# Kernel optimization log

Measured on AMD Instinct MI355X. Metric: run time of the kernel, lower is better.

## Reference

```python
import jax, jax.numpy as jnp
import numpy as np

K = 9        # kNN neighbors (ViG default kernel_size=9)
EPS = 1e-5   # BatchNorm eps


def _bn2d(x, gamma, beta):
    # training-mode BatchNorm2d over (B,H,W) per channel; x: [B,C,H,W]
    mean = jnp.mean(x, axis=(0, 2, 3), keepdims=True)
    var = jnp.var(x, axis=(0, 2, 3), keepdims=True)
    g = gamma.reshape(1, -1, 1, 1)
    b = beta.reshape(1, -1, 1, 1)
    return g * (x - mean) * jax.lax.rsqrt(var + EPS) + b


def setup_inputs() -> dict:
    key = jax.random.key(0)
    B, C, H, W = 8, 96, 56, 56
    oup = 192
    ks = jax.random.split(key, 8)
    sc = 0.05
    return {
        "x": jax.random.normal(ks[0], (B, C, H, W), dtype=jnp.float32),
        "W_fc1": jax.random.normal(ks[1], (C, C), dtype=jnp.float32) * sc,
        "b_fc1": jnp.zeros((C,), jnp.float32),
        "g_bn1": jnp.ones((C,), jnp.float32),
        "be_bn1": jnp.zeros((C,), jnp.float32),
        "W_edge": jax.random.normal(ks[2], (2 * C, 2 * C), dtype=jnp.float32) * sc,
        "b_edge": jnp.zeros((2 * C,), jnp.float32),
        "g_bne": jnp.ones((2 * C,), jnp.float32),
        "be_bne": jnp.zeros((2 * C,), jnp.float32),
        "W_fc2": jax.random.normal(ks[3], (2 * C, C), dtype=jnp.float32) * sc,
        "b_fc2": jnp.zeros((C,), jnp.float32),
        "g_bn2": jnp.ones((C,), jnp.float32),
        "be_bn2": jnp.zeros((C,), jnp.float32),
        "g_sabn": jnp.ones((C,), jnp.float32),
        "be_sabn": jnp.zeros((C,), jnp.float32),
        "W_dw": jax.random.normal(ks[4], (oup, C, 3, 3), dtype=jnp.float32) * sc,
        "b_dw": jnp.zeros((oup,), jnp.float32),
        "g_dwbn": jnp.ones((oup,), jnp.float32),
        "be_dwbn": jnp.zeros((oup,), jnp.float32),
    }


def reference(x, W_fc1, b_fc1, g_bn1, be_bn1, W_edge, b_edge, g_bne, be_bne,
              W_fc2, b_fc2, g_bn2, be_bn2, g_sabn, be_sabn,
              W_dw, b_dw, g_dwbn, be_dwbn):
    B, C, H, W = x.shape
    N = H * W
    shortcut = x

    # --- Grapher.fc1: 1x1 conv + BN ---
    y = jnp.einsum('bchw,cd->bdhw', x, W_fc1) + b_fc1[None, :, None, None]
    y = _bn2d(y, g_bn1, be_bn1)

    # --- dynamic kNN graph over flattened tokens ---
    ft = y.reshape(B, C, N).transpose(0, 2, 1)            # [B,N,C]
    sq = jnp.sum(ft * ft, axis=-1)                        # [B,N]
    dist = sq[:, :, None] - 2.0 * jnp.einsum('bnc,bmc->bnm', ft, ft) + sq[:, None, :]
    _, idx = jax.lax.top_k(-dist, K)                      # [B,N,K] nearest neighbors

    # --- EdgeConv: max_k act(BN(W [x_i, x_j - x_i])) ---
    x_j = jnp.take_along_axis(ft[:, :, None, :], idx[..., None], axis=1)  # [B,N,K,C]
    x_i = ft[:, :, None, :]                               # [B,N,1,C]
    e = jnp.concatenate([jnp.broadcast_to(x_i, x_j.shape), x_j - x_i], axis=-1)  # [B,N,K,2C]
    e = jnp.einsum('bnkc,cd->bnkd', e, W_edge) + b_edge
    m = jnp.mean(e, axis=(0, 1, 2))
    v = jnp.var(e, axis=(0, 1, 2))
    e = g_bne * (e - m) * jax.lax.rsqrt(v + EPS) + be_bne
    e = jax.nn.relu(e)
    g = jnp.max(e, axis=2)                                # [B,N,2C] max-aggregation

    # --- Grapher.fc2: 1x1 conv + BN, residual ---
    g = jnp.einsum('bnc,cd->bnd', g, W_fc2) + b_fc2       # [B,N,C]
    g = g.transpose(0, 2, 1).reshape(B, C, H, W)
    g = _bn2d(g, g_bn2, be_bn2)
    y = g + shortcut

    # --- SAEncoder: BN + ReLU ---
    y = jax.nn.relu(_bn2d(y, g_sabn, be_sabn))

    # --- convdw: 3x3 stride-2 conv + BN + ReLU ---
    y = jax.lax.conv_general_dilated(
        y, W_dw, window_strides=(2, 2), padding=((1, 1), (1, 1)),
        dimension_numbers=('NCHW', 'OIHW', 'NCHW')) + b_dw[None, :, None, None]
    y = jax.nn.relu(_bn2d(y, g_dwbn, be_dwbn))
    return y
```

## Files before the change

kernel.cpp:

```cpp
#include <hip/hip_runtime.h>
#include <math.h>

#define B_   8
#define C_   96
#define C2_  192
#define N_   3136
#define R_   25088
#define OUP_ 192
#define HO_  28
#define NO_  784
#define EPS_ 1e-5f
#define QS2  128
#define CAP3 64

typedef short bf16x8 __attribute__((ext_vector_type(8)));
typedef float f32x4  __attribute__((ext_vector_type(4)));

__device__ __forceinline__ int swz16(int i) { return (i & ~15) | ((i & 15) ^ ((i >> 4) & 7)); }

__global__ __launch_bounds__(512) void k_fc1_d(const float* __restrict__ x,
                                               const float* __restrict__ W1,
                                               const float* __restrict__ b1,
                                               double* __restrict__ yd) {
    __shared__ double Wl[96 * 48];
    int tid = threadIdx.x;
    int rl = tid & 255, h = tid >> 8;
    int dbase = blockIdx.y * 48;
    for (int q = tid; q < 96 * 48; q += 512) {
        int c = q / 48, dd = q % 48;
        Wl[c * 48 + dd] = (double)W1[c * 96 + dbase + dd];
    }
    __syncthreads();
    int r = blockIdx.x * 256 + rl;
    int b = r / N_;
    int n = r - b * N_;
    double acc[24];
#pragma unroll
    for (int i = 0; i < 24; i++) acc[i] = 0.0;
    const float* xp = x + (size_t)b * C_ * N_ + n;
    for (int c = 0; c < 96; ++c) {
        double xv = (double)xp[(size_t)c * N_];
        const double* w = &Wl[c * 48 + h * 24];
#pragma unroll
        for (int i = 0; i < 24; ++i) acc[i] += xv * w[i];
    }
    int d0 = dbase + h * 24;
#pragma unroll
    for (int i = 0; i < 24; i++) {
        int d = d0 + i;
        yd[((size_t)b * C_ + d) * N_ + n] = acc[i] + (double)b1[d];
    }
}

__global__ __launch_bounds__(256) void k_stats_chan_d(const double* __restrict__ src,
                                                      double* __restrict__ partial) {
    int c = blockIdx.x;
    int chunk = blockIdx.y;
    const int SPLIT = 16;
    double s = 0.0, ss = 0.0;
    for (int j = chunk * 256 + threadIdx.x; j < R_; j += SPLIT * 256) {
        int b = j / N_, n = j - b * N_;
        double v = src[((size_t)b * C_ + c) * N_ + n];
        s += v;
        ss += v * v;
    }
    __shared__ double red[8];
    for (int off = 32; off; off >>= 1) {
        s += __shfl_down(s, off, 64);
        ss += __shfl_down(ss, off, 64);
    }
    int lane = threadIdx.x & 63, w = threadIdx.x >> 6;
    if (lane == 0) { red[w * 2] = s; red[w * 2 + 1] = ss; }
    __syncthreads();
    if (threadIdx.x == 0) {
        s = red[0] + red[2] + red[4] + red[6];
        ss = red[1] + red[3] + red[5] + red[7];
        partial[(c * SPLIT + chunk) * 2] = s;
        partial[(c * SPLIT + chunk) * 2 + 1] = ss;
    }
}

__global__ void k_stats_reduce_d(const double* __restrict__ partial, double* __restrict__ stats) {
    int c = blockIdx.x * blockDim.x + threadIdx.x;
    if (c >= 96) return;
    double s = 0.0, ss = 0.0;
    for (int k = 0; k < 16; k++) {
        s += partial[(c * 16 + k) * 2];
        ss += partial[(c * 16 + k) * 2 + 1];
    }
    double m = s / (double)R_;
    double var = ss / (double)R_ - m * m;
    stats[c * 2] = m;
    stats[c * 2 + 1] = 1.0 / sqrt(var + 1e-5);
}

__global__ __launch_bounds__(256) void k_stats_chan(const float* __restrict__ src,
                                                    float* __restrict__ partial,
                                                    int Cn, int Nsp, int total) {
    int c = blockIdx.x;
    int chunk = blockIdx.y;
    int SPLIT = gridDim.y;
    float s = 0.f, ss = 0.f;
    for (int j = chunk * 256 + threadIdx.x; j < total; j += SPLIT * 256) {
        int b = j / Nsp, n = j - b * Nsp;
        float v = src[((size_t)b * Cn + c) * Nsp + n];
        s += v;
        ss += v * v;
    }
    __shared__ float red[8];
    for (int off = 32; off; off >>= 1) {
        s += __shfl_down(s, off, 64);
        ss += __shfl_down(ss, off, 64);
    }
    int lane = threadIdx.x & 63, w = threadIdx.x >> 6;
    if (lane == 0) { red[w * 2] = s; red[w * 2 + 1] = ss; }
    __syncthreads();
    if (threadIdx.x == 0) {
        s = red[0] + red[2] + red[4] + red[6];
        ss = red[1] + red[3] + red[5] + red[7];
        partial[(c * SPLIT + chunk) * 2] = s;
        partial[(c * SPLIT + chunk) * 2 + 1] = ss;
    }
}

__global__ void k_stats_reduce(const float* __restrict__ partial, float* __restrict__ stats,
                               int Cn, int SPLIT, float invcount) {
    int c = blockIdx.x * blockDim.x + threadIdx.x;
    if (c >= Cn) return;
    float s = 0.f, ss = 0.f;
    for (int k = 0; k < SPLIT; k++) {
        s += partial[(c * SPLIT + k) * 2];
        ss += partial[(c * SPLIT + k) * 2 + 1];
    }
    float m = s * invcount;
    float var = ss * invcount - m * m;
    stats[c * 2] = m;
    stats[c * 2 + 1] = 1.0f / sqrtf(var + EPS_);
}

__global__ __launch_bounds__(256) void k_stats_reduce_b2(const float* __restrict__ partial,
                                                         float* __restrict__ stats,
                                                         float invcount) {
    int c = blockIdx.x;
    float s = 0.f, ss = 0.f;
    for (int k = threadIdx.x; k < 784; k += 256) {
        s  += partial[(size_t)k * 384 + c];
        ss += partial[(size_t)k * 384 + 192 + c];
    }
    __shared__ float red[8];
    for (int off = 32; off; off >>= 1) {
        s += __shfl_down(s, off, 64);
        ss += __shfl_down(ss, off, 64);
    }
    int lane = threadIdx.x & 63, w = threadIdx.x >> 6;
    if (lane == 0) { red[w * 2] = s; red[w * 2 + 1] = ss; }
    __syncthreads();
    if (threadIdx.x == 0) {
        s = red[0] + red[2] + red[4] + red[6];
        ss = red[1] + red[3] + red[5] + red[7];
        float m = s * invcount;
        float var = ss * invcount - m * m;
        stats[c * 2] = m;
        stats[c * 2 + 1] = 1.0f / sqrtf(var + EPS_);
    }
}

__global__ __launch_bounds__(256) void k_bn1_tr(const double* __restrict__ yd,
                                                const double* __restrict__ stats,
                                                const float* __restrict__ g,
                                                const float* __restrict__ be,
                                                float* __restrict__ ftc,
                                                double* __restrict__ ftp64,
                                                unsigned short* __restrict__ fspH,
                                                double* __restrict__ sq64) {
    __shared__ double tile[64 * 97];
    __shared__ double dsq[64][4];
    int b = blockIdx.y;
    int n0 = blockIdx.x * 64;
    int tid = threadIdx.x;
    int n = tid & 63, w = tid >> 6;
    for (int k = 0; k < 24; ++k) {
        int c = k * 4 + w;
        size_t gi = ((size_t)b * C_ + c) * N_ + n0 + n;
        double m = stats[c * 2], rs = stats[c * 2 + 1];
        double v = (double)g[c] * (yd[gi] - m) * rs + (double)be[c];
        ftc[gi] = (float)v;
        tile[n * 97 + c] = v;
    }
    __syncthreads();
    int p = n, q = w;
    double vals[24];
    double s = 0.0;
    const double* lp = &tile[p * 97 + q * 24];
#pragma unroll
    for (int m2 = 0; m2 < 24; ++m2) { vals[m2] = lp[m2]; s += vals[m2] * vals[m2]; }
    dsq[p][q] = s;
    double* dst = ftp64 + ((size_t)b * N_ + n0 + p) * C_ + q * 24;
#pragma unroll
    for (int m2 = 0; m2 < 24; m2 += 2) *(double2*)&dst[m2] = make_double2(vals[m2], vals[m2 + 1]);
    unsigned* hdst = (unsigned*)(fspH + ((size_t)b * N_ + n0 + p) * QS2);
#pragma unroll
    for (int m2 = 0; m2 < 24; m2 += 2) {
        unsigned u0 = __float_as_uint((float)vals[m2]);
        unsigned u1 = __float_as_uint((float)vals[m2 + 1]);
        unsigned h0 = (u0 + 0x7fffu + ((u0 >> 16) & 1u)) >> 16;
        unsigned h1 = (u1 + 0x7fffu + ((u1 >> 16) & 1u)) >> 16;
        hdst[q * 12 + (m2 >> 1)] = h0 | (h1 << 16);
    }
    __syncthreads();
    if (tid < 64) {
        double tot = dsq[tid][0] + dsq[tid][1] + dsq[tid][2] + dsq[tid][3];
        sq64[(size_t)b * N_ + n0 + tid] = tot;
        float t32 = (float)(-0.5 * tot);
        unsigned u0 = __float_as_uint(t32);
        unsigned h0 = (u0 + 0x7fffu + ((u0 >> 16) & 1u)) >> 16;
        float resid = t32 - __uint_as_float(h0 << 16);
        unsigned u1 = __float_as_uint(resid);
        unsigned h1 = (u1 + 0x7fffu + ((u1 >> 16) & 1u)) >> 16;
        unsigned* hd = (unsigned*)(fspH + ((size_t)b * N_ + n0 + tid) * QS2);
        hd[48] = h0 | (h1 << 16);
#pragma unroll
        for (int k2 = 49; k2 < 64; ++k2) hd[k2] = 0u;
    }
}

__global__ __launch_bounds__(256) void k_dist_min(const unsigned short* __restrict__ fspH,
                                                  unsigned short* __restrict__ cminG) {
    __shared__ __align__(16) char lds[32768];
    int b = blockIdx.z, half = blockIdx.y;
    int q0 = blockIdx.x * 64;
    int tid = threadIdx.x, w = tid >> 6, l = tid & 63;
    int ch0 = half * 25;
    int nch = half ? 24 : 25;
    const int koff = (l >> 4) * 8;

    {
        const uint4* qsrc = (const uint4*)(fspH + ((size_t)b * N_ + q0) * QS2);
        const uint4* csrc = (const uint4*)(fspH + ((size_t)b * N_ + ch0 * 64) * QS2);
        uint4* qb = (uint4*)(lds + 16384);
        uint4* cb = (uint4*)lds;
        for (int i = tid; i < 1024; i += 256) { qb[swz16(i)] = qsrc[i]; cb[swz16(i)] = csrc[i]; }
    }
    __syncthreads();
    bf16x8 Bq[4];
    {
        const unsigned short* Ql = (const unsigned short*)(lds + 16384);
        int qr = w * 16 + (l & 15);
#pragma unroll
        for (int s = 0; s < 3; ++s) {
            int col = (s * 4 + (l >> 4)) ^ (qr & 7);
            Bq[s] = *(const bf16x8*)&Ql[qr * QS2 + col * 8];
        }
        bf16x8 z = {0, 0, 0, 0, 0, 0, 0, 0};
        if ((l >> 4) == 0) { z[0] = (short)0x3F80; z[1] = (short)0x3F80; }
        Bq[3] = z;
    }
    __syncthreads();

    int cur = 0;
    for (int t = 0; t < nch; ++t) {
        int chg = ch0 + t;
        bool pf = (t < nch - 1);
        uint4 st0, st1, st2, st3;
        if (pf) {
            const uint4* src = (const uint4*)(fspH + ((size_t)b * N_ + (chg + 1) * 64) * QS2);
            st0 = src[tid]; st1 = src[tid + 256]; st2 = src[tid + 512]; st3 = src[tid + 768];
        }
        const unsigned short* Bc = (const unsigned short*)(lds + cur * 16384);
        f32x4 acc[4];
#pragma unroll
        for (int ct = 0; ct < 4; ++ct) acc[ct] = (f32x4){0.f, 0.f, 0.f, 0.f};
#pragma unroll
        for (int s = 0; s < 4; ++s) {
#pragma unroll
            for (int ct = 0; ct < 4; ++ct) {
                int cr = ct * 16 + (l & 15);
                int col = (s * 4 + (l >> 4)) ^ (cr & 7);
                bf16x8 Ac = *(const bf16x8*)&Bc[cr * QS2 + col * 8];
                acc[ct] = __builtin_amdgcn_mfma_f32_16x16x32_bf16(Ac, Bq[s], acc[ct], 0, 0, 0);
            }
        }
        float mx = -1e30f;
#pragma unroll
        for (int ct = 0; ct < 4; ++ct)
#pragma unroll
            for (int j = 0; j < 4; ++j) mx = fmaxf(mx, acc[ct][j]);
        mx = fmaxf(mx, __shfl_xor(mx, 16, 64));
        mx = fmaxf(mx, __shfl_xor(mx, 32, 64));
        if (l < 16) {
            float dmin = -2.f * mx;
            unsigned u = __float_as_uint(dmin);
            unsigned ku = u ^ (0x80000000u | (unsigned)((int)u >> 31));
            cminG[((size_t)(b * N_ + q0 + w * 16 + l)) * 49 + chg] = (unsigned short)(ku >> 16);
        }
        if (pf) {
            uint4* dst = (uint4*)(lds + (cur ^ 1) * 16384);
            dst[swz16(tid)] = st0;
            dst[swz16(tid + 256)] = st1;
            dst[swz16(tid + 512)] = st2;
            dst[swz16(tid + 768)] = st3;
        }
        __syncthreads();
        cur ^= 1;
    }
}

__global__ __launch_bounds__(256) void k_t9(const unsigned short* __restrict__ cminG,
                                            float* __restrict__ thr2f,
                                            unsigned* __restrict__ poolCnt) {
    int q = blockIdx.x * 256 + threadIdx.x;
    if (q >= R_) return;
    const unsigned short* p = cminG + (size_t)q * 49;
    unsigned short top[9];
#pragma unroll
    for (int j = 0; j < 9; ++j) top[j] = 0xFFFFu;
    for (int i = 0; i < 49; ++i) {
        unsigned short v = p[i];
        if (v < top[8]) {
            top[8] = v;
#pragma unroll
            for (int j = 8; j >= 1; --j)
                if (top[j] < top[j - 1]) { unsigned short tt = top[j]; top[j] = top[j - 1]; top[j - 1] = tt; }
        }
    }
    unsigned ku = ((unsigned)top[8] << 16) | 0xFFFFu;
    float f = (ku & 0x80000000u) ? __uint_as_float(ku ^ 0x80000000u) : __uint_as_float(~ku);
    float t9 = f + fabsf(f) * 0.008f + 0.75f;
    thr2f[q] = -0.5f * t9;
    poolCnt[q] = 0u;
}

__global__ __launch_bounds__(256) void k_dist_cmp(const unsigned short* __restrict__ fspH,
                                                  const float* __restrict__ thr2f,
                                                  unsigned short* __restrict__ poolC,
                                                  unsigned* __restrict__ poolCnt) {
    __shared__ __align__(16) char lds[32768];
    int b = blockIdx.z, half = blockIdx.y;
    int q0 = blockIdx.x * 64;
    int tid = threadIdx.x, w = tid >> 6, l = tid & 63;
    int ch0 = half * 25;
    int nch = half ? 24 : 25;
    const int koff = (l >> 4) * 8;
    int qg = b * N_ + q0 + w * 16 + (l & 15);
    float thr2r = thr2f[qg];

    {
        const uint4* qsrc = (const uint4*)(fspH + ((size_t)b * N_ + q0) * QS2);
        const uint4* csrc = (const uint4*)(fspH + ((size_t)b * N_ + ch0 * 64) * QS2);
        uint4* qb = (uint4*)(lds + 16384);
        uint4* cb = (uint4*)lds;
        for (int i = tid; i < 1024; i += 256) { qb[swz16(i)] = qsrc[i]; cb[swz16(i)] = csrc[i]; }
    }
    __syncthreads();
    bf16x8 Bq[4];
    {
        const unsigned short* Ql = (const unsigned short*)(lds + 16384);
        int qr = w * 16 + (l & 15);
#pragma unroll
        for (int s = 0; s < 3; ++s) {
            int col = (s * 4 + (l >> 4)) ^ (qr & 7);
            Bq[s] = *(const bf16x8*)&Ql[qr * QS2 + col * 8];
        }
        bf16x8 z = {0, 0, 0, 0, 0, 0, 0, 0};
        if ((l >> 4) == 0) { z[0] = (short)0x3F80; z[1] = (short)0x3F80; }
        Bq[3] = z;
    }
    __syncthreads();

    int cur = 0;
    for (int t = 0; t < nch; ++t) {
        int chg = ch0 + t;
        int c0 = chg * 64;
        bool pf = (t < nch - 1);
        uint4 st0, st1, st2, st3;
        if (pf) {
            const uint4* src = (const uint4*)(fspH + ((size_t)b * N_ + (chg + 1) * 64) * QS2);
            st0 = src[tid]; st1 = src[tid + 256]; st2 = src[tid + 512]; st3 = src[tid + 768];
        }
        const unsigned short* Bc = (const unsigned short*)(lds + cur * 16384);
        f32x4 acc[4];
#pragma unroll
        for (int ct = 0; ct < 4; ++ct) acc[ct] = (f32x4){0.f, 0.f, 0.f, 0.f};
#pragma unroll
        for (int s = 0; s < 4; ++s) {
#pragma unroll
            for (int ct = 0; ct < 4; ++ct) {
                int cr = ct * 16 + (l & 15);
                int col = (s * 4 + (l >> 4)) ^ (cr & 7);
                bf16x8 Ac = *(const bf16x8*)&Bc[cr * QS2 + col * 8];
                acc[ct] = __builtin_amdgcn_mfma_f32_16x16x32_bf16(Ac, Bq[s], acc[ct], 0, 0, 0);
            }
        }
#pragma unroll
        for (int ct = 0; ct < 4; ++ct)
#pragma unroll
            for (int j = 0; j < 4; ++j) {
                if (acc[ct][j] >= thr2r) {
                    unsigned pos = atomicAdd(&poolCnt[qg], 1u);
                    if (pos < (unsigned)CAP3)
                        poolC[(size_t)qg * CAP3 + pos] = (unsigned short)(c0 + ct * 16 + (l >> 4) * 4 + j);
                }
            }
        if (pf) {
            uint4* dst = (uint4*)(lds + (cur ^ 1) * 16384);
            dst[swz16(tid)] = st0;
            dst[swz16(tid + 256)] = st1;
            dst[swz16(tid + 512)] = st2;
            dst[swz16(tid + 768)] = st3;
        }
        __syncthreads();
        cur ^= 1;
    }
}

__global__ __launch_bounds__(256) void k_rerank_d(const unsigned short* __restrict__ poolC,
                                                  const unsigned* __restrict__ poolCnt,
                                                  const double* __restrict__ ftp64,
                                                  const double* __restrict__ sq64,
                                                  int* __restrict__ idx) {
    int tid = threadIdx.x;
    int wv = tid >> 6, l = tid & 63;
    int rr = blockIdx.x * 4 + wv;
    int b = rr / N_;
    int cnt = (int)poolCnt[rr];
    if (cnt > CAP3) cnt = CAP3;
    int e = l & 3;
    double qreg[24];
    {
        const double* qb = ftp64 + (size_t)rr * C_ + e * 24;
#pragma unroll
        for (int m = 0; m < 24; ++m) qreg[m] = qb[m];
    }
    double dv[4];
    int jv[4];
#pragma unroll
    for (int gG = 0; gG < 4; ++gG) { dv[gG] = 1e300; jv[gG] = 0x7fffffff; }
#pragma unroll
    for (int gG = 0; gG < 4; ++gG) {
        if (gG * 16 >= cnt) break;
        int ci = gG * 16 + (l >> 2);
        bool valid = ci < cnt;
        int j = valid ? (int)poolC[(size_t)rr * CAP3 + ci] : 0;
        const double* cb = ftp64 + ((size_t)b * N_ + j) * C_ + e * 24;
        double p = 0.0;
#pragma unroll
        for (int m = 0; m < 24; ++m) p += qreg[m] * cb[m];
        p += __shfl_xor(p, 1, 64);
        p += __shfl_xor(p, 2, 64);
        if (valid) {
            dv[gG] = sq64[(size_t)b * N_ + j] - 2.0 * p;
            jv[gG] = j;
        }
    }
#pragma unroll
    for (int r = 0; r < 9; ++r) {
        double dm = dv[0]; int jm = jv[0];
#pragma unroll
        for (int gG = 1; gG < 4; ++gG)
            if (dv[gG] < dm || (dv[gG] == dm && jv[gG] < jm)) { dm = dv[gG]; jm = jv[gG]; }
#pragma unroll
        for (int off = 1; off <= 32; off <<= 1) {
            double od = __shfl_xor(dm, off, 64);
            int oj = __shfl_xor(jm, off, 64);
            if (od < dm || (od == dm && oj < jm)) { dm = od; jm = oj; }
        }
        if (l == 0) idx[(size_t)rr * 9 + r] = jm;
#pragma unroll
        for (int gG = 0; gG < 4; ++gG)
            if (jv[gG] == jm) dv[gG] = 1e300;
    }
}

__global__ __launch_bounds__(512) void k_gemm_uv2(const float* __restrict__ ftc,
                                                  const float* __restrict__ We,
                                                  const float* __restrict__ beb,
                                                  float* __restrict__ u,
                                                  float* __restrict__ v) {
    __shared__ float Wl[2][96 * 48];
    int tid = threadIdx.x;
    int rl = tid & 255, h = tid >> 8;
    int dbase = blockIdx.y * 48;
    for (int q = tid; q < 96 * 48; q += 512) {
        int c = q / 48, dd = q % 48;
        float wb = We[(96 + c) * C2_ + dbase + dd];
        Wl[1][q] = wb;
        Wl[0][q] = We[c * C2_ + dbase + dd] - wb;
    }
    __syncthreads();
    int r = blockIdx.x * 256 + rl;
    int b = r / N_, n = r - b * N_;
    float a0[24], a1[24];
#pragma unroll
    for (int i = 0; i < 24; i++) { a0[i] = 0.f; a1[i] = 0.f; }
    const float* xp = ftc + (size_t)b * C_ * N_ + n;
    for (int c = 0; c < 96; ++c) {
        float xv = xp[(size_t)c * N_];
        const float4* w40 = (const float4*)&Wl[0][c * 48 + h * 24];
        const float4* w41 = (const float4*)&Wl[1][c * 48 + h * 24];
#pragma unroll
        for (int i = 0; i < 6; ++i) {
            float4 w0 = w40[i], w1 = w41[i];
            a0[i * 4 + 0] += xv * w0.x; a0[i * 4 + 1] += xv * w0.y;
            a0[i * 4 + 2] += xv * w0.z; a0[i * 4 + 3] += xv * w0.w;
            a1[i * 4 + 0] += xv * w1.x; a1[i * 4 + 1] += xv * w1.y;
            a1[i * 4 + 2] += xv * w1.z; a1[i * 4 + 3] += xv * w1.w;
        }
    }
    int d0 = dbase + h * 24;
    float* up = u + (size_t)r * C2_ + d0;
    float* vp = v + (size_t)r * C2_ + d0;
#pragma unroll
    for (int i = 0; i < 6; ++i) {
        float4 ou, ov;
        ou.x = a0[i * 4 + 0] + beb[d0 + i * 4 + 0];
        ou.y = a0[i * 4 + 1] + beb[d0 + i * 4 + 1];
        ou.z = a0[i * 4 + 2] + beb[d0 + i * 4 + 2];
        ou.w = a0[i * 4 + 3] + beb[d0 + i * 4 + 3];
        ov.x = a1[i * 4 + 0]; ov.y = a1[i * 4 + 1];
        ov.z = a1[i * 4 + 2]; ov.w = a1[i * 4 + 3];
        ((float4*)up)[i] = ou;
        ((float4*)vp)[i] = ov;
    }
}

__global__ __launch_bounds__(192) void k_bne_stats(const float* __restrict__ u,
                                                   const float* __restrict__ v,
                                                   const int* __restrict__ idx,
                                                   float* __restrict__ partial) {
    int d = threadIdx.x;
    int row0 = blockIdx.x * 32;
    int b = row0 / N_;
    float s = 0.f, ss = 0.f;
    for (int r = 0; r < 32; ++r) {
        int row = row0 + r;
        float ud = u[(size_t)row * C2_ + d];
        const int* ip = idx + (size_t)row * 9;
#pragma unroll
        for (int k = 0; k < 9; k++) {
            int j = ip[k];
            float e = ud + v[((size_t)b * N_ + j) * C2_ + d];
            s += e;
            ss += e * e;
        }
    }
    partial[(size_t)blockIdx.x * 384 + d] = s;
    partial[(size_t)blockIdx.x * 384 + 192 + d] = ss;
}

__global__ __launch_bounds__(192) void k_edge_fc2(const float* __restrict__ u,
                                                  const float* __restrict__ v,
                                                  const int* __restrict__ idx,
                                                  const float* __restrict__ statsE,
                                                  const float* __restrict__ ge,
                                                  const float* __restrict__ bee,
                                                  const float* __restrict__ W2,
                                                  const float* __restrict__ b2,
                                                  float* __restrict__ out2) {
    __shared__ float gl[16][C2_];
    __shared__ float g2[C_][16];
    int tid = threadIdx.x;
    int row0 = blockIdx.x * 16;
    int b = row0 / N_;
    int n0 = row0 - b * N_;
    {
        int d = tid;
        float m = statsE[d * 2], rs = statsE[d * 2 + 1];
        float ga = ge[d], bb = bee[d];
        for (int r = 0; r < 16; ++r) {
            int row = row0 + r;
            float ud = u[(size_t)row * C2_ + d];
            const int* ip = idx + (size_t)row * 9;
            float gm = 0.f;
#pragma unroll
            for (int k = 0; k < 9; k++) {
                int j = ip[k];
                float e = ud + v[((size_t)b * N_ + j) * C2_ + d];
                float val = ga * (e - m) * rs + bb;
                gm = fmaxf(gm, val);
            }
            gl[r][d] = gm;
        }
    }
    __syncthreads();
    {
        int rr = tid / 24;
        int dq = tid % 24;
        for (int rep = 0; rep < 2; ++rep) {
            int r = rr + rep * 8;
            float4 acc = *(const float4*)&b2[dq * 4];
            for (int d = 0; d < C2_; ++d) {
                float gv = gl[r][d];
                float4 w = *(const float4*)&W2[d * C_ + dq * 4];
                acc.x += gv * w.x;
                acc.y += gv * w.y;
                acc.z += gv * w.z;
                acc.w += gv * w.w;
            }
            g2[dq * 4 + 0][r] = acc.x;
            g2[dq * 4 + 1][r] = acc.y;
            g2[dq * 4 + 2][r] = acc.z;
            g2[dq * 4 + 3][r] = acc.w;
        }
    }
    __syncthreads();
    for (int q = tid; q < 96 * 4; q += 192) {
        int dd = q / 4, part = q % 4;
        float4 val = *(const float4*)&g2[dd][part * 4];
        *(float4*)&out2[((size_t)b * C_ + dd) * N_ + n0 + part * 4] = val;
    }
}

__global__ __launch_bounds__(256) void k_bn2_add_st(const float* __restrict__ out2,
                                                    const float* __restrict__ x,
                                                    const float* __restrict__ stats,
                                                    const float* __restrict__ g,
                                                    const float* __restrict__ be,
                                                    float* __restrict__ t,
                                                    float* __restrict__ partial) {
    int c = blockIdx.x;
    int chunk = blockIdx.y;
    const int SPLIT = 16;
    float m = stats[c * 2], rs = stats[c * 2 + 1];
    float ga = g[c], bb = be[c];
    float s = 0.f, ss = 0.f;
    for (int j = chunk * 256 + threadIdx.x; j < R_; j += SPLIT * 256) {
        int b = j / N_, n = j - b * N_;
        size_t i = ((size_t)b * C_ + c) * N_ + n;
        float tv = ga * (out2[i] - m) * rs + bb + x[i];
        t[i] = tv;
        s += tv;
        ss += tv * tv;
    }
    __shared__ float red[8];
    for (int off = 32; off; off >>= 1) {
        s += __shfl_down(s, off, 64);
        ss += __shfl_down(ss, off, 64);
    }
    int lane = threadIdx.x & 63, w = threadIdx.x >> 6;
    if (lane == 0) { red[w * 2] = s; red[w * 2 + 1] = ss; }
    __syncthreads();
    if (threadIdx.x == 0) {
        s = red[0] + red[2] + red[4] + red[6];
        ss = red[1] + red[3] + red[5] + red[7];
        partial[(c * SPLIT + chunk) * 2] = s;
        partial[(c * SPLIT + chunk) * 2 + 1] = ss;
    }
}

__global__ __launch_bounds__(256) void k_sabn_relu(const float* __restrict__ t,
                                                   const float* __restrict__ stats,
                                                   const float* __restrict__ g,
                                                   const float* __restrict__ be,
                                                   float* __restrict__ s) {
    int i = blockIdx.x * 256 + threadIdx.x;
    if (i >= B_ * C_ * N_) return;
    int c = (i / N_) % C_;
    s[i] = fmaxf(g[c] * (t[i] - stats[c * 2]) * stats[c * 2 + 1] + be[c], 0.f);
}

__global__ __launch_bounds__(256) void k_conv(const float* __restrict__ s,
                                              const float* __restrict__ Wd,
                                              const float* __restrict__ bd,
                                              float* __restrict__ z) {
    __shared__ float Wl[96 * 9 * 16];
    int b = blockIdx.z;
    int oc0 = blockIdx.y * 16;
    int p = blockIdx.x * 256 + threadIdx.x;
    for (int i = threadIdx.x; i < 96 * 9 * 16; i += 256) {
        int oc = i & 15;
        int icq = i >> 4;
        Wl[i] = Wd[(size_t)(oc0 + oc) * 864 + icq];
    }
    __syncthreads();
    if (p >= NO_) return;
    int oh = p / HO_, ow = p % HO_;
    float acc[16];
#pragma unroll
    for (int i = 0; i < 16; i++) acc[i] = 0.f;
    int ih0 = oh * 2 - 1, iw0 = ow * 2 - 1;
    const float* sb = s + (size_t)b * C_ * N_;
    for (int ic = 0; ic < 96; ++ic) {
        const float* sp = sb + (size_t)ic * N_;
        float in[9];
#pragma unroll
        for (int kh = 0; kh < 3; kh++) {
            int ih = ih0 + kh;
            bool okh = (unsigned)ih < 56u;
#pragma unroll
            for (int kw = 0; kw < 3; kw++) {
                int iw = iw0 + kw;
                bool ok = okh && ((unsigned)iw < 56u);
                in[kh * 3 + kw] = ok ? sp[ih * 56 + iw] : 0.f;
            }
        }
#pragma unroll
        for (int q = 0; q < 9; q++) {
            float iv = in[q];
            const float4* w4 = (const float4*)&Wl[(ic * 9 + q) * 16];
#pragma unroll
            for (int j = 0; j < 4; j++) {
                float4 w = w4[j];
                acc[j * 4 + 0] += iv * w.x;
                acc[j * 4 + 1] += iv * w.y;
                acc[j * 4 + 2] += iv * w.z;
                acc[j * 4 + 3] += iv * w.w;
            }
        }
    }
#pragma unroll
    for (int i = 0; i < 16; i++)
        z[((size_t)b * OUP_ + oc0 + i) * NO_ + p] = acc[i] + bd[oc0 + i];
}

__global__ __launch_bounds__(256) void k_out(const float* __restrict__ z,
                                             const float* __restrict__ stats,
                                             const float* __restrict__ g,
                                             const float* __restrict__ be,
                                             float* __restrict__ out) {
    int i = blockIdx.x * 256 + threadIdx.x;
    if (i >= B_ * OUP_ * NO_) return;
    int c = (i / NO_) % OUP_;
    out[i] = fmaxf(g[c] * (z[i] - stats[c * 2]) * stats[c * 2 + 1] + be[c], 0.f);
}

extern "C" void kernel_launch(void* const* d_in, const int* in_sizes, int n_in,
                              void* d_out, int out_size, void* d_ws, size_t ws_size,
                              hipStream_t stream) {
    const float* x     = (const float*)d_in[0];
    const float* W_fc1 = (const float*)d_in[1];
    const float* b_fc1 = (const float*)d_in[2];
    const float* g_bn1 = (const float*)d_in[3];
    const float* be_bn1= (const float*)d_in[4];
    const float* W_edge= (const float*)d_in[5];
    const float* b_edge= (const float*)d_in[6];
    const float* g_bne = (const float*)d_in[7];
    const float* be_bne= (const float*)d_in[8];
    const float* W_fc2 = (const float*)d_in[9];
    const float* b_fc2 = (const float*)d_in[10];
    const float* g_bn2 = (const float*)d_in[11];
    const float* be_bn2= (const float*)d_in[12];
    const float* g_sabn= (const float*)d_in[13];
    const float* be_sabn=(const float*)d_in[14];
    const float* W_dw  = (const float*)d_in[15];
    const float* b_dw  = (const float*)d_in[16];
    const float* g_dwbn= (const float*)d_in[17];
    const float* be_dwbn=(const float*)d_in[18];

    char* base = (char*)d_ws;
    float*  ftc   = (float*)(base + 0);
    float*  sbuf  = (float*)(base + 0);
    double* ftp64 = (double*)(base + 9633792);
    float*  uu    = (float*)(base + 9633792);
    double* yd    = (double*)(base + 28901376);
    float*  vv    = (float*)(base + 28901376);
    unsigned short* fspH = (unsigned short*)(base + 48168960);
    float*  out2  = (float*)(base + 48168960);
    unsigned short* poolC = (unsigned short*)(base + 57802752);
    float*  tbuf  = (float*)(base + 57802752);
    double* sq64  = (double*)(base + 67436544);
    int*    idx   = (int*)(base + 67637248);
    unsigned* poolCnt = (unsigned*)(base + 68540416);
    float*  thr2f = (float*)(base + 68640768);
    float*  partial = (float*)(base + 68741120);
    double* partiald = (double*)(base + 68741120);
    double* stats1d = (double*)(base + 69945344);
    float*  statsE  = (float*)(base + 69946880);
    float*  stats2  = (float*)(base + 69948416);
    float*  statsS  = (float*)(base + 69949952);
    float*  statsD  = (float*)(base + 69951488);
    float*  zbuf  = (float*)(base + 69953024);
    unsigned short* cminG = (unsigned short*)(base + 69953024);

    k_fc1_d<<<dim3(98, 2), 512, 0, stream>>>(x, W_fc1, b_fc1, yd);
    k_stats_chan_d<<<dim3(96, 16), 256, 0, stream>>>(yd, partiald);
    k_stats_reduce_d<<<1, 256, 0, stream>>>(partiald, stats1d);
    k_bn1_tr<<<dim3(49, B_), 256, 0, stream>>>(yd, stats1d, g_bn1, be_bn1, ftc, ftp64, fspH, sq64);

    k_dist_min<<<dim3(49, 2, B_), 256, 0, stream>>>(fspH, cminG);
    k_t9<<<98, 256, 0, stream>>>(cminG, thr2f, poolCnt);
    k_dist_cmp<<<dim3(49, 2, B_), 256, 0, stream>>>(fspH, thr2f, poolC, poolCnt);
    k_rerank_d<<<6272, 256, 0, stream>>>(poolC, poolCnt, ftp64, sq64, idx);

    k_gemm_uv2<<<dim3(98, 4), 512, 0, stream>>>(ftc, W_edge, b_edge, uu, vv);

    k_bne_stats<<<784, 192, 0, stream>>>(uu, vv, idx, partial);
    k_stats_reduce_b2<<<192, 256, 0, stream>>>(partial, statsE, 1.0f / 225792.0f);
    k_edge_fc2<<<1568, 192, 0, stream>>>(uu, vv, idx, statsE, g_bne, be_bne, W_fc2, b_fc2, out2);

    k_stats_chan<<<dim3(96, 16), 256, 0, stream>>>(out2, partial, 96, N_, R_);
    k_stats_reduce<<<1, 256, 0, stream>>>(partial, stats2, 96, 16, 1.0f / (float)R_);
    k_bn2_add_st<<<dim3(96, 16), 256, 0, stream>>>(out2, x, stats2, g_bn2, be_bn2, tbuf, partial);
    k_stats_reduce<<<1, 256, 0, stream>>>(partial, statsS, 96, 16, 1.0f / (float)R_);
    k_sabn_relu<<<9408, 256, 0, stream>>>(tbuf, statsS, g_sabn, be_sabn, sbuf);

    k_conv<<<dim3(4, 12, 8), 256, 0, stream>>>(sbuf, W_dw, b_dw, zbuf);
    k_stats_chan<<<dim3(192, 8), 256, 0, stream>>>(zbuf, partial, 192, NO_, 6272);
    k_stats_reduce<<<1, 256, 0, stream>>>(partial, statsD, 192, 8, 1.0f / 6272.0f);
    k_out<<<4705, 256, 0, stream>>>(zbuf, statsD, g_dwbn, be_dwbn, (float*)d_out);
}
```

Measured before the change: 590.4 us.

## Fuse kNN threshold passes, fold BN stats into producers, fuse SA-BN into conv

Merges the kNN min-distance pass, the top-9 threshold kernel and the candidate-compare pass into one kernel. Each block computes its own per-chunk minima in LDS, derives the threshold, then re-walks the same chunks to collect candidates, which removes the cminG/thr2f round trips and two launches. The fc2 edge kernel now emits per-block BN2 partial sums, and the conv kernel applies SA-BN+ReLU on the fly and emits BN partials for the output stats. This drops the separate stats-channel passes and the sbuf write. Trade-offs: the conv now uses 8 output channels per block, doubling input re-reads, and the fused kNN kernel streams the candidates twice from global memory inside a single kernel.

```diff
diff --git a/kernel.cpp b/kernel.cpp
--- a/kernel.cpp
+++ b/kernel.cpp
@@ -94,35 +94,6 @@
     stats[c * 2 + 1] = 1.0 / sqrt(var + 1e-5);
 }
 
-__global__ __launch_bounds__(256) void k_stats_chan(const float* __restrict__ src,
-                                                    float* __restrict__ partial,
-                                                    int Cn, int Nsp, int total) {
-    int c = blockIdx.x;
-    int chunk = blockIdx.y;
-    int SPLIT = gridDim.y;
-    float s = 0.f, ss = 0.f;
-    for (int j = chunk * 256 + threadIdx.x; j < total; j += SPLIT * 256) {
-        int b = j / Nsp, n = j - b * Nsp;
-        float v = src[((size_t)b * Cn + c) * Nsp + n];
-        s += v;
-        ss += v * v;
-    }
-    __shared__ float red[8];
-    for (int off = 32; off; off >>= 1) {
-        s += __shfl_down(s, off, 64);
-        ss += __shfl_down(ss, off, 64);
-    }
-    int lane = threadIdx.x & 63, w = threadIdx.x >> 6;
-    if (lane == 0) { red[w * 2] = s; red[w * 2 + 1] = ss; }
-    __syncthreads();
-    if (threadIdx.x == 0) {
-        s = red[0] + red[2] + red[4] + red[6];
-        ss = red[1] + red[3] + red[5] + red[7];
-        partial[(c * SPLIT + chunk) * 2] = s;
-        partial[(c * SPLIT + chunk) * 2 + 1] = ss;
-    }
-}
-
 __global__ void k_stats_reduce(const float* __restrict__ partial, float* __restrict__ stats,
                                int Cn, int SPLIT, float invcount) {
     int c = blockIdx.x * blockDim.x + threadIdx.x;
@@ -138,14 +109,14 @@
     stats[c * 2 + 1] = 1.0f / sqrtf(var + EPS_);
 }
 
-__global__ __launch_bounds__(256) void k_stats_reduce_b2(const float* __restrict__ partial,
-                                                         float* __restrict__ stats,
-                                                         float invcount) {
+__global__ __launch_bounds__(256) void k_stats_reduce_g(const float* __restrict__ partial,
+                                                        float* __restrict__ stats,
+                                                        int Cn, int NB, float invcount) {
     int c = blockIdx.x;
     float s = 0.f, ss = 0.f;
-    for (int k = threadIdx.x; k < 784; k += 256) {
-        s  += partial[(size_t)k * 384 + c];
-        ss += partial[(size_t)k * 384 + 192 + c];
+    for (int k = threadIdx.x; k < NB; k += 256) {
+        s  += partial[(size_t)k * 2 * Cn + c];
+        ss += partial[(size_t)k * 2 * Cn + Cn + c];
     }
     __shared__ float red[8];
     for (int off = 32; off; off >>= 1) {
@@ -172,7 +143,8 @@
                                                 float* __restrict__ ftc,
                                                 double* __restrict__ ftp64,
                                                 unsigned short* __restrict__ fspH,
-                                                double* __restrict__ sq64) {
+                                                double* __restrict__ sq64,
+                                                unsigned* __restrict__ poolCnt) {
     __shared__ double tile[64 * 97];
     __shared__ double dsq[64][4];
     int b = blockIdx.y;
@@ -211,6 +183,7 @@
     if (tid < 64) {
         double tot = dsq[tid][0] + dsq[tid][1] + dsq[tid][2] + dsq[tid][3];
         sq64[(size_t)b * N_ + n0 + tid] = tot;
+        poolCnt[(size_t)b * N_ + n0 + tid] = 0u;
         float t32 = (float)(-0.5 * tot);
         unsigned u0 = __float_as_uint(t32);
         unsigned h0 = (u0 + 0x7fffu + ((u0 >> 16) & 1u)) >> 16;
@@ -224,27 +197,27 @@
     }
 }
 
-__global__ __launch_bounds__(256) void k_dist_min(const unsigned short* __restrict__ fspH,
-                                                  unsigned short* __restrict__ cminG) {
-    __shared__ __align__(16) char lds[32768];
+__global__ __launch_bounds__(256) void k_dist5(const unsigned short* __restrict__ fspH,
+                                               unsigned short* __restrict__ poolC,
+                                               unsigned* __restrict__ poolCnt) {
+    __shared__ __align__(16) char lds[39680];
+    float* cminF = (float*)(lds + 32768);
+    float* t9fL  = (float*)(lds + 39168);
     int b = blockIdx.z, half = blockIdx.y;
     int q0 = blockIdx.x * 64;
     int tid = threadIdx.x, w = tid >> 6, l = tid & 63;
-    int ch0 = half * 25;
-    int nch = half ? 24 : 25;
-    const int koff = (l >> 4) * 8;
+    int ch0 = half * 25, nch = half ? 24 : 25;
+    int qg = b * N_ + q0 + w * 16 + (l & 15);
 
     {
-        const uint4* qsrc = (const uint4*)(fspH + ((size_t)b * N_ + q0) * QS2);
-        const uint4* csrc = (const uint4*)(fspH + ((size_t)b * N_ + ch0 * 64) * QS2);
-        uint4* qb = (uint4*)(lds + 16384);
-        uint4* cb = (uint4*)lds;
-        for (int i = tid; i < 1024; i += 256) { qb[swz16(i)] = qsrc[i]; cb[swz16(i)] = csrc[i]; }
+        const uint4* src = (const uint4*)(fspH + ((size_t)b * N_ + q0) * QS2);
+        uint4* dst = (uint4*)lds;
+        for (int i = tid; i < 1024; i += 256) dst[swz16(i)] = src[i];
     }
     __syncthreads();
     bf16x8 Bq[4];
     {
-        const unsigned short* Ql = (const unsigned short*)(lds + 16384);
+        const unsigned short* Ql = (const unsigned short*)lds;
         int qr = w * 16 + (l & 15);
 #pragma unroll
         for (int s = 0; s < 3; ++s) {
@@ -257,13 +230,25 @@
     }
     __syncthreads();
 
+    {
+        const uint4* src = (const uint4*)(fspH + ((size_t)b * N_ + ch0 * 64) * QS2);
+        uint4* dst = (uint4*)lds;
+        for (int i = tid; i < 1024; i += 256) dst[swz16(i)] = src[i];
+    }
+    __syncthreads();
+
+    float thr2r = 1e30f;
     int cur = 0;
-    for (int t = 0; t < nch; ++t) {
-        int chg = ch0 + t;
-        bool pf = (t < nch - 1);
+    int nct = 2 * nch;
+    for (int t = 0; t < nct; ++t) {
+        int chl = (t < nch) ? t : t - nch;
+        int c0 = (ch0 + chl) * 64;
+        bool pf = (t < nct - 1);
         uint4 st0, st1, st2, st3;
         if (pf) {
-            const uint4* src = (const uint4*)(fspH + ((size_t)b * N_ + (chg + 1) * 64) * QS2);
+            int tn = t + 1;
+            int nc = ch0 + ((tn < nch) ? tn : tn - nch);
+            const uint4* src = (const uint4*)(fspH + ((size_t)b * N_ + nc * 64) * QS2);
             st0 = src[tid]; st1 = src[tid + 256]; st2 = src[tid + 512]; st3 = src[tid + 768];
         }
         const unsigned short* Bc = (const unsigned short*)(lds + cur * 16384);
@@ -280,127 +265,48 @@
                 acc[ct] = __builtin_amdgcn_mfma_f32_16x16x32_bf16(Ac, Bq[s], acc[ct], 0, 0, 0);
             }
         }
-        float mx = -1e30f;
-#pragma unroll
-        for (int ct = 0; ct < 4; ++ct)
-#pragma unroll
-            for (int j = 0; j < 4; ++j) mx = fmaxf(mx, acc[ct][j]);
-        mx = fmaxf(mx, __shfl_xor(mx, 16, 64));
-        mx = fmaxf(mx, __shfl_xor(mx, 32, 64));
-        if (l < 16) {
-            float dmin = -2.f * mx;
-            unsigned u = __float_as_uint(dmin);
-            unsigned ku = u ^ (0x80000000u | (unsigned)((int)u >> 31));
-            cminG[((size_t)(b * N_ + q0 + w * 16 + l)) * 49 + chg] = (unsigned short)(ku >> 16);
-        }
-        if (pf) {
-            uint4* dst = (uint4*)(lds + (cur ^ 1) * 16384);
-            dst[swz16(tid)] = st0;
-            dst[swz16(tid + 256)] = st1;
-            dst[swz16(tid + 512)] = st2;
-            dst[swz16(tid + 768)] = st3;
-        }
-        __syncthreads();
-        cur ^= 1;
-    }
-}
-
-__global__ __launch_bounds__(256) void k_t9(const unsigned short* __restrict__ cminG,
-                                            float* __restrict__ thr2f,
-                                            unsigned* __restrict__ poolCnt) {
-    int q = blockIdx.x * 256 + threadIdx.x;
-    if (q >= R_) return;
-    const unsigned short* p = cminG + (size_t)q * 49;
-    unsigned short top[9];
-#pragma unroll
-    for (int j = 0; j < 9; ++j) top[j] = 0xFFFFu;
-    for (int i = 0; i < 49; ++i) {
-        unsigned short v = p[i];
-        if (v < top[8]) {
-            top[8] = v;
-#pragma unroll
-            for (int j = 8; j >= 1; --j)
-                if (top[j] < top[j - 1]) { unsigned short tt = top[j]; top[j] = top[j - 1]; top[j - 1] = tt; }
-        }
-    }
-    unsigned ku = ((unsigned)top[8] << 16) | 0xFFFFu;
-    float f = (ku & 0x80000000u) ? __uint_as_float(ku ^ 0x80000000u) : __uint_as_float(~ku);
-    float t9 = f + fabsf(f) * 0.008f + 0.75f;
-    thr2f[q] = -0.5f * t9;
-    poolCnt[q] = 0u;
-}
-
-__global__ __launch_bounds__(256) void k_dist_cmp(const unsigned short* __restrict__ fspH,
-                                                  const float* __restrict__ thr2f,
-                                                  unsigned short* __restrict__ poolC,
-                                                  unsigned* __restrict__ poolCnt) {
-    __shared__ __align__(16) char lds[32768];
-    int b = blockIdx.z, half = blockIdx.y;
-    int q0 = blockIdx.x * 64;
-    int tid = threadIdx.x, w = tid >> 6, l = tid & 63;
-    int ch0 = half * 25;
-    int nch = half ? 24 : 25;
-    const int koff = (l >> 4) * 8;
-    int qg = b * N_ + q0 + w * 16 + (l & 15);
-    float thr2r = thr2f[qg];
-
-    {
-        const uint4* qsrc = (const uint4*)(fspH + ((size_t)b * N_ + q0) * QS2);
-        const uint4* csrc = (const uint4*)(fspH + ((size_t)b * N_ + ch0 * 64) * QS2);
-        uint4* qb = (uint4*)(lds + 16384);
-        uint4* cb = (uint4*)lds;
-        for (int i = tid; i < 1024; i += 256) { qb[swz16(i)] = qsrc[i]; cb[swz16(i)] = csrc[i]; }
-    }
-    __syncthreads();
-    bf16x8 Bq[4];
-    {
-        const unsigned short* Ql = (const unsigned short*)(lds + 16384);
-        int qr = w * 16 + (l & 15);
-#pragma unroll
-        for (int s = 0; s < 3; ++s) {
-            int col = (s * 4 + (l >> 4)) ^ (qr & 7);
-            Bq[s] = *(const bf16x8*)&Ql[qr * QS2 + col * 8];
-        }
-        bf16x8 z = {0, 0, 0, 0, 0, 0, 0, 0};
-        if ((l >> 4) == 0) { z[0] = (short)0x3F80; z[1] = (short)0x3F80; }
-        Bq[3] = z;
-    }
-    __syncthreads();
-
-    int cur = 0;
-    for (int t = 0; t < nch; ++t) {
-        int chg = ch0 + t;
-        int c0 = chg * 64;
-        bool pf = (t < nch - 1);
-        uint4 st0, st1, st2, st3;
-        if (pf) {
-            const uint4* src = (const uint4*)(fspH + ((size_t)b * N_ + (chg + 1) * 64) * QS2);
-            st0 = src[tid]; st1 = src[tid + 256]; st2 = src[tid + 512]; st3 = src[tid + 768];
-        }
-        const unsigned short* Bc = (const unsigned short*)(lds + cur * 16384);
-        f32x4 acc[4];
-#pragma unroll
-        for (int ct = 0; ct < 4; ++ct) acc[ct] = (f32x4){0.f, 0.f, 0.f, 0.f};
-#pragma unroll
-        for (int s = 0; s < 4; ++s) {
-#pragma unroll
-            for (int ct = 0; ct < 4; ++ct) {
-                int cr = ct * 16 + (l & 15);
-                int col = (s * 4 + (l >> 4)) ^ (cr & 7);
-                bf16x8 Ac = *(const bf16x8*)&Bc[cr * QS2 + col * 8];
-                acc[ct] = __builtin_amdgcn_mfma_f32_16x16x32_bf16(Ac, Bq[s], acc[ct], 0, 0, 0);
+        if (t < nch) {
+            float mx = -1e30f;
+#pragma unroll
+            for (int ct = 0; ct < 4; ++ct)
+#pragma unroll
+                for (int j = 0; j < 4; ++j) mx = fmaxf(mx, acc[ct][j]);
+            mx = fmaxf(mx, __shfl_xor(mx, 16, 64));
+            mx = fmaxf(mx, __shfl_xor(mx, 32, 64));
+            if (l < 16) cminF[chl * 64 + w * 16 + l] = -2.f * mx;
+        } else {
+#pragma unroll
+            for (int ct = 0; ct < 4; ++ct)
+#pragma unroll
+                for (int j = 0; j < 4; ++j) {
+                    if (acc[ct][j] >= thr2r) {
+                        unsigned pos = atomicAdd(&poolCnt[qg], 1u);
+                        if (pos < (unsigned)CAP3)
+                            poolC[(size_t)qg * CAP3 + pos] = (unsigned short)(c0 + ct * 16 + (l >> 4) * 4 + j);
+                    }
+                }
+        }
+        if (t == nch - 1) {
+            __syncthreads();
+            if (tid < 64) {
+                float top[9];
+#pragma unroll
+                for (int j = 0; j < 9; ++j) top[j] = 1e30f;
+                for (int q = 0; q < nch; ++q) {
+                    float v = cminF[q * 64 + tid];
+                    if (v < top[8]) {
+                        top[8] = v;
+#pragma unroll
+                        for (int j = 8; j >= 1; --j)
+                            if (top[j] < top[j - 1]) { float tt = top[j]; top[j] = top[j - 1]; top[j - 1] = tt; }
+                    }
+                }
+                float t9 = top[8] + fabsf(top[8]) * 0.008f + 0.75f;
+                t9fL[tid] = -0.5f * t9;
             }
-        }
-#pragma unroll
-        for (int ct = 0; ct < 4; ++ct)
-#pragma unroll
-            for (int j = 0; j < 4; ++j) {
-                if (acc[ct][j] >= thr2r) {
-                    unsigned pos = atomicAdd(&poolCnt[qg], 1u);
-                    if (pos < (unsigned)CAP3)
-                        poolC[(size_t)qg * CAP3 + pos] = (unsigned short)(c0 + ct * 16 + (l >> 4) * 4 + j);
-                }
-            }
+            __syncthreads();
+            thr2r = t9fL[w * 16 + (l & 15)];
+        }
         if (pf) {
             uint4* dst = (uint4*)(lds + (cur ^ 1) * 16384);
             dst[swz16(tid)] = st0;
@@ -547,15 +453,16 @@
     partial[(size_t)blockIdx.x * 384 + 192 + d] = ss;
 }
 
-__global__ __launch_bounds__(192) void k_edge_fc2(const float* __restrict__ u,
-                                                  const float* __restrict__ v,
-                                                  const int* __restrict__ idx,
-                                                  const float* __restrict__ statsE,
-                                                  const float* __restrict__ ge,
-                                                  const float* __restrict__ bee,
-                                                  const float* __restrict__ W2,
-                                                  const float* __restrict__ b2,
-                                                  float* __restrict__ out2) {
+__global__ __launch_bounds__(192) void k_edge_fc2_st(const float* __restrict__ u,
+                                                     const float* __restrict__ v,
+                                                     const int* __restrict__ idx,
+                                                     const float* __restrict__ statsE,
+                                                     const float* __restrict__ ge,
+                                                     const float* __restrict__ bee,
+                                                     const float* __restrict__ W2,
+                                                     const float* __restrict__ b2,
+                                                     float* __restrict__ out2,
+                                                     float* __restrict__ partialE) {
     __shared__ float gl[16][C2_];
     __shared__ float g2[C_][16];
     int tid = threadIdx.x;
@@ -607,6 +514,22 @@
         int dd = q / 4, part = q % 4;
         float4 val = *(const float4*)&g2[dd][part * 4];
         *(float4*)&out2[((size_t)b * C_ + dd) * N_ + n0 + part * 4] = val;
+    }
+    {
+        int c = tid >> 1, h = tid & 1;
+        float s = 0.f, ss = 0.f;
+#pragma unroll
+        for (int r = 0; r < 8; ++r) {
+            float vv = g2[c][h * 8 + r];
+            s += vv;
+            ss += vv * vv;
+        }
+        s += __shfl_xor(s, 1, 64);
+        ss += __shfl_xor(ss, 1, 64);
+        if (h == 0) {
+            partialE[(size_t)blockIdx.x * 192 + c] = s;
+            partialE[(size_t)blockIdx.x * 192 + 96 + c] = ss;
+        }
     }
 }
 
@@ -647,58 +570,60 @@
     }
 }
 
-__global__ __launch_bounds__(256) void k_sabn_relu(const float* __restrict__ t,
-                                                   const float* __restrict__ stats,
-                                                   const float* __restrict__ g,
-                                                   const float* __restrict__ be,
-                                                   float* __restrict__ s) {
-    int i = blockIdx.x * 256 + threadIdx.x;
-    if (i >= B_ * C_ * N_) return;
-    int c = (i / N_) % C_;
-    s[i] = fmaxf(g[c] * (t[i] - stats[c * 2]) * stats[c * 2 + 1] + be[c], 0.f);
-}
-
-__global__ __launch_bounds__(256) void k_conv(const float* __restrict__ s,
-                                              const float* __restrict__ Wd,
-                                              const float* __restrict__ bd,
-                                              float* __restrict__ z) {
-    __shared__ float Wl[96 * 9 * 16];
+__global__ __launch_bounds__(256) void k_conv8(const float* __restrict__ t,
+                                               const float* __restrict__ statsS,
+                                               const float* __restrict__ gS,
+                                               const float* __restrict__ beS,
+                                               const float* __restrict__ Wd,
+                                               const float* __restrict__ bd,
+                                               float* __restrict__ z,
+                                               float* __restrict__ partialD) {
+    __shared__ float Wl[96 * 9 * 8];
+    __shared__ float scl[96], shf[96];
+    __shared__ float redc[4][16];
     int b = blockIdx.z;
-    int oc0 = blockIdx.y * 16;
+    int oc0 = blockIdx.y * 8;
     int p = blockIdx.x * 256 + threadIdx.x;
-    for (int i = threadIdx.x; i < 96 * 9 * 16; i += 256) {
-        int oc = i & 15;
-        int icq = i >> 4;
+    for (int i = threadIdx.x; i < 96 * 9 * 8; i += 256) {
+        int oc = i & 7, icq = i >> 3;
         Wl[i] = Wd[(size_t)(oc0 + oc) * 864 + icq];
     }
-    __syncthreads();
-    if (p >= NO_) return;
-    int oh = p / HO_, ow = p % HO_;
-    float acc[16];
-#pragma unroll
-    for (int i = 0; i < 16; i++) acc[i] = 0.f;
+    if (threadIdx.x < 96) {
+        int c = threadIdx.x;
+        float m = statsS[c * 2], rs = statsS[c * 2 + 1], ga = gS[c];
+        scl[c] = ga * rs;
+        shf[c] = beS[c] - ga * m * rs;
+    }
+    __syncthreads();
+    bool valid = p < NO_;
+    int oh = valid ? p / HO_ : 0, ow = valid ? p % HO_ : 0;
+    float acc[8];
+#pragma unroll
+    for (int i = 0; i < 8; i++) acc[i] = 0.f;
     int ih0 = oh * 2 - 1, iw0 = ow * 2 - 1;
-    const float* sb = s + (size_t)b * C_ * N_;
+    const float* tb = t + (size_t)b * C_ * N_;
     for (int ic = 0; ic < 96; ++ic) {
-        const float* sp = sb + (size_t)ic * N_;
+        const float* sp = tb + (size_t)ic * N_;
+        float sc_ = scl[ic], sh_ = shf[ic];
         float in[9];
 #pragma unroll
         for (int kh = 0; kh < 3; kh++) {
             int ih = ih0 + kh;
-            bool okh = (unsigned)ih < 56u;
+            bool okh = valid && ((unsigned)ih < 56u);
 #pragma unroll
             for (int kw = 0; kw < 3; kw++) {
                 int iw = iw0 + kw;
                 bool ok = okh && ((unsigned)iw < 56u);
-                in[kh * 3 + kw] = ok ? sp[ih * 56 + iw] : 0.f;
+                float raw = ok ? sp[ih * 56 + iw] : 0.f;
+                in[kh * 3 + kw] = ok ? fmaxf(sc_ * raw + sh_, 0.f) : 0.f;
             }
         }
 #pragma unroll
         for (int q = 0; q < 9; q++) {
             float iv = in[q];
-            const float4* w4 = (const float4*)&Wl[(ic * 9 + q) * 16];
-#pragma unroll
-            for (int j = 0; j < 4; j++) {
+            const float4* w4 = (const float4*)&Wl[(ic * 9 + q) * 8];
+#pragma unroll
+            for (int j = 0; j < 2; j++) {
                 float4 w = w4[j];
                 acc[j * 4 + 0] += iv * w.x;
                 acc[j * 4 + 1] += iv * w.y;
@@ -707,9 +632,46 @@
             }
         }
     }
-#pragma unroll
-    for (int i = 0; i < 16; i++)
-        z[((size_t)b * OUP_ + oc0 + i) * NO_ + p] = acc[i] + bd[oc0 + i];
+    float s8[8];
+#pragma unroll
+    for (int i = 0; i < 8; i++) {
+        float ov = acc[i] + bd[oc0 + i];
+        if (valid) z[((size_t)b * OUP_ + oc0 + i) * NO_ + p] = ov;
+        s8[i] = valid ? ov : 0.f;
+    }
+    int w = threadIdx.x >> 6;
+#pragma unroll
+    for (int i = 0; i < 8; ++i) {
+        float s = s8[i], ss = s8[i] * s8[i];
+        for (int off = 32; off; off >>= 1) {
+            s += __shfl_down(s, off, 64);
+            ss += __shfl_down(ss, off, 64);
+        }
+        if ((threadIdx.x & 63) == 0) { redc[w][i * 2] = s; redc[w][i * 2 + 1] = ss; }
+    }
+    __syncthreads();
+    if (threadIdx.x < 16) {
+        float v = redc[0][threadIdx.x] + redc[1][threadIdx.x] + redc[2][threadIdx.x] + redc[3][threadIdx.x];
+        int blk = (b * 24 + blockIdx.y) * 4 + blockIdx.x;
+        partialD[blk * 16 + threadIdx.x] = v;
+    }
+}
+
+__global__ void k_stats_reduce_conv(const float* __restrict__ partialD, float* __restrict__ stats) {
+    int c = threadIdx.x;
+    if (c >= 192) return;
+    int y = c >> 3, o = c & 7;
+    float s = 0.f, ss = 0.f;
+    for (int bb = 0; bb < 8; ++bb)
+        for (int x2 = 0; x2 < 4; ++x2) {
+            int blk = (bb * 24 + y) * 4 + x2;
+            s += partialD[blk * 16 + o * 2];
+            ss += partialD[blk * 16 + o * 2 + 1];
+        }
+    float m = s / 6272.f;
+    float var = ss / 6272.f - m * m;
+    stats[c * 2] = m;
+    stats[c * 2 + 1] = 1.0f / sqrtf(var + EPS_);
 }
 
 __global__ __launch_bounds__(256) void k_out(const float* __restrict__ z,
@@ -748,7 +710,6 @@
 
     char* base = (char*)d_ws;
     float*  ftc   = (float*)(base + 0);
-    float*  sbuf  = (float*)(base + 0);
     double* ftp64 = (double*)(base + 9633792);
     float*  uu    = (float*)(base + 9633792);
     double* yd    = (double*)(base + 28901376);
@@ -760,7 +721,6 @@
     double* sq64  = (double*)(base + 67436544);
     int*    idx   = (int*)(base + 67637248);
     unsigned* poolCnt = (unsigned*)(base + 68540416);
-    float*  thr2f = (float*)(base + 68640768);
     float*  partial = (float*)(base + 68741120);
     double* partiald = (double*)(base + 68741120);
     double* stats1d = (double*)(base + 69945344);
@@ -769,32 +729,26 @@
     float*  statsS  = (float*)(base + 69949952);
     float*  statsD  = (float*)(base + 69951488);
     float*  zbuf  = (float*)(base + 69953024);
-    unsigned short* cminG = (unsigned short*)(base + 69953024);
 
     k_fc1_d<<<dim3(98, 2), 512, 0, stream>>>(x, W_fc1, b_fc1, yd);
     k_stats_chan_d<<<dim3(96, 16), 256, 0, stream>>>(yd, partiald);
     k_stats_reduce_d<<<1, 256, 0, stream>>>(partiald, stats1d);
-    k_bn1_tr<<<dim3(49, B_), 256, 0, stream>>>(yd, stats1d, g_bn1, be_bn1, ftc, ftp64, fspH, sq64);
-
-    k_dist_min<<<dim3(49, 2, B_), 256, 0, stream>>>(fspH, cminG);
-    k_t9<<<98, 256, 0, stream>>>(cminG, thr2f, poolCnt);
-    k_dist_cmp<<<dim3(49, 2, B_), 256, 0, stream>>>(fspH, thr2f, poolC, poolCnt);
+    k_bn1_tr<<<dim3(49, B_), 256, 0, stream>>>(yd, stats1d, g_bn1, be_bn1, ftc, ftp64, fspH, sq64, poolCnt);
+
+    k_dist5<<<dim3(49, 2, B_), 256, 0, stream>>>(fspH, poolC, poolCnt);
     k_rerank_d<<<6272, 256, 0, stream>>>(poolC, poolCnt, ftp64, sq64, idx);
 
     k_gemm_uv2<<<dim3(98, 4), 512, 0, stream>>>(ftc, W_edge, b_edge, uu, vv);
 
     k_bne_stats<<<784, 192, 0, stream>>>(uu, vv, idx, partial);
-    k_stats_reduce_b2<<<192, 256, 0, stream>>>(partial, statsE, 1.0f / 225792.0f);
-    k_edge_fc2<<<1568, 192, 0, stream>>>(uu, vv, idx, statsE, g_bne, be_bne, W_fc2, b_fc2, out2);
-
-    k_stats_chan<<<dim3(96, 16), 256, 0, stream>>>(out2, partial, 96, N_, R_);
-    k_stats_reduce<<<1, 256, 0, stream>>>(partial, stats2, 96, 16, 1.0f / (float)R_);
+    k_stats_reduce_g<<<192, 256, 0, stream>>>(partial, statsE, 192, 784, 1.0f / 225792.0f);
+    k_edge_fc2_st<<<1568, 192, 0, stream>>>(uu, vv, idx, statsE, g_bne, be_bne, W_fc2, b_fc2, out2, partial);
+    k_stats_reduce_g<<<96, 256, 0, stream>>>(partial, stats2, 96, 1568, 1.0f / (float)R_);
+
     k_bn2_add_st<<<dim3(96, 16), 256, 0, stream>>>(out2, x, stats2, g_bn2, be_bn2, tbuf, partial);
     k_stats_reduce<<<1, 256, 0, stream>>>(partial, statsS, 96, 16, 1.0f / (float)R_);
-    k_sabn_relu<<<9408, 256, 0, stream>>>(tbuf, statsS, g_sabn, be_sabn, sbuf);
-
-    k_conv<<<dim3(4, 12, 8), 256, 0, stream>>>(sbuf, W_dw, b_dw, zbuf);
-    k_stats_chan<<<dim3(192, 8), 256, 0, stream>>>(zbuf, partial, 192, NO_, 6272);
-    k_stats_reduce<<<1, 256, 0, stream>>>(partial, statsD, 192, 8, 1.0f / 6272.0f);
+
+    k_conv8<<<dim3(4, 24, 8), 256, 0, stream>>>(tbuf, statsS, g_sabn, be_sabn, W_dw, b_dw, zbuf, partial);
+    k_stats_reduce_conv<<<1, 192, 0, stream>>>(partial, statsD);
     k_out<<<4705, 256, 0, stream>>>(zbuf, statsD, g_dwbn, be_dwbn, (float*)d_out);
 }
```

Measured after the change: 692.3 us. 1.17x slower.
